# Kernel optimization log

Hardware: AMD Instinct MI355X
Metric: run time of the kernel (lower is better)

The kernel has to match this reference:

```python
import jax, jax.numpy as jnp
import numpy as np

N_ATOMS = 100_000
N_BONDS = 200_000
MAX_NB = 6
HIDDEN = 300
ATOM_FD = 133
BOND_FD = 147
DEPTH = 3
ATOMS_PER_MOL = 20
N_MOLS = N_ATOMS // ATOMS_PER_MOL


def setup_inputs() -> dict:
    key = jax.random.key(0)
    ks = jax.random.split(key, 9)
    f_atoms = jax.random.normal(ks[0], (N_ATOMS, ATOM_FD), dtype=jnp.float32)
    f_bonds = jax.random.normal(ks[1], (N_BONDS, BOND_FD), dtype=jnp.float32)
    a2b = jax.random.randint(ks[2], (N_ATOMS, MAX_NB), 0, N_BONDS, dtype=jnp.int32)
    b2a = jax.random.randint(ks[3], (N_BONDS,), 0, N_ATOMS, dtype=jnp.int32)
    b2revb = jax.random.randint(ks[4], (N_BONDS,), 0, N_BONDS, dtype=jnp.int32)
    mol_ids = (jnp.arange(N_ATOMS, dtype=jnp.int32) // ATOMS_PER_MOL).astype(jnp.int32)
    W_i = jax.random.normal(ks[5], (BOND_FD, HIDDEN), dtype=jnp.float32) * 0.05
    W_h = jax.random.normal(ks[6], (HIDDEN, HIDDEN), dtype=jnp.float32) * 0.05
    W_o = jax.random.normal(ks[7], (ATOM_FD + HIDDEN, HIDDEN), dtype=jnp.float32) * 0.05
    b_o = jax.random.normal(ks[8], (HIDDEN,), dtype=jnp.float32) * 0.05
    return {"f_atoms": f_atoms, "f_bonds": f_bonds, "a2b": a2b, "b2a": b2a,
            "b2revb": b2revb, "mol_ids": mol_ids, "W_i": W_i, "W_h": W_h,
            "W_o": W_o, "b_o": b_o}


def reference(f_atoms, f_bonds, a2b, b2a, b2revb, mol_ids, W_i, W_h, W_o, b_o):
    # input = W_i(f_bonds); message = act(input)
    inp = f_bonds @ W_i                     # [n_bonds, H]
    message = jax.nn.relu(inp)
    for _ in range(DEPTH - 1):
        # padded-neighbor gather + sum over incoming bonds per atom
        a_message = message[a2b].sum(axis=1)          # [n_atoms, H]
        # forward gather minus reverse-bond message
        m = a_message[b2a] - message[b2revb]          # [n_bonds, H]
        message = jax.nn.relu(inp + m @ W_h)          # (dropout p=0 omitted)
    # final atom readout
    a_message = message[a2b].sum(axis=1)              # [n_atoms, H]
    a_input = jnp.concatenate([f_atoms, a_message], axis=1)  # [n_atoms, atom_fd+H]
    atom_hiddens = jax.nn.relu(a_input @ W_o + b_o)   # [n_atoms, H]
    # 'mean' pooling over each molecule's atoms (contiguous equal-size scopes)
    mol_sums = jax.ops.segment_sum(atom_hiddens, mol_ids, num_segments=N_MOLS)
    return mol_sums / ATOMS_PER_MOL                   # [n_mols, H]
```

## Files before the change

### kernel.cpp

```cpp
#include <hip/hip_runtime.h>
#include <hip/hip_bf16.h>
#include <hip/hip_fp8.h>

#define N_ATOMS 100000
#define N_BONDS 200000
#define MAX_NB 6
#define HIDDEN 300
#define HP 320
#define CH 40
#define ATOM_FD 133
#define BOND_FD 147
#define N_MOLS 5000
#define APM 20

#define NT32 10
#define KKI32 10
#define KKH32 20
#define KKO32 28

using bf16 = __hip_bfloat16;
typedef __attribute__((ext_vector_type(8))) short short8v;
typedef __attribute__((ext_vector_type(4))) float float4v;
typedef __attribute__((ext_vector_type(2))) float float2v;
typedef __attribute__((ext_vector_type(16))) float float16v;
typedef unsigned int u32;
typedef unsigned short u16;
typedef unsigned char u8;

__device__ __forceinline__ float us2f(u16 u) {
    union { u32 i; float f; } v; v.i = ((u32)u) << 16; return v.f;
}
__device__ __forceinline__ u16 f2us(float f) {
    bf16 h = __float2bfloat16(f);
    return *(u16*)&h;
}
__device__ __forceinline__ u32 pack2(float a, float b) {
    return (u32)f2us(a) | ((u32)f2us(b) << 16);
}
__device__ __forceinline__ uint2 pack4(const float4v& a) {
    uint2 o; o.x = pack2(a[0], a[1]); o.y = pack2(a[2], a[3]); return o;
}

#if defined(__has_builtin)
#if __has_builtin(__builtin_amdgcn_cvt_f32_fp8) && __has_builtin(__builtin_amdgcn_cvt_pk_fp8_f32)
#define HW_FP8 1
#endif
#if __has_builtin(__builtin_amdgcn_cvt_pk_f32_fp8)
#define HW_FP8_PK 1
#endif
#endif

__device__ __forceinline__ void f8x4_to_f32(u32 p, float* o) {
#if defined(HW_FP8_PK)
    float2v lo = __builtin_amdgcn_cvt_pk_f32_fp8(p, false);
    float2v hi = __builtin_amdgcn_cvt_pk_f32_fp8(p, true);
    o[0] = lo[0]; o[1] = lo[1]; o[2] = hi[0]; o[3] = hi[1];
#elif defined(HW_FP8)
    o[0] = __builtin_amdgcn_cvt_f32_fp8(p, 0);
    o[1] = __builtin_amdgcn_cvt_f32_fp8(p, 1);
    o[2] = __builtin_amdgcn_cvt_f32_fp8(p, 2);
    o[3] = __builtin_amdgcn_cvt_f32_fp8(p, 3);
#else
#pragma unroll
    for (int i = 0; i < 4; ++i) {
        __hip_fp8_e4m3 h; h.__x = (u8)(p >> (8 * i));
        o[i] = (float)h;
    }
#endif
}
__device__ __forceinline__ u32 f32x4_to_f8(float a, float b, float c, float d) {
#ifdef HW_FP8
    u32 r = __builtin_amdgcn_cvt_pk_fp8_f32(a, b, 0u, false);
    r = __builtin_amdgcn_cvt_pk_fp8_f32(c, d, r, true);
    return r;
#else
    __hip_fp8_e4m3 ha(a), hb(b), hc(c), hd(d);
    return (u32)ha.__x | ((u32)hb.__x << 8) | ((u32)hc.__x << 16) | ((u32)hd.__x << 24);
#endif
}
__device__ __forceinline__ void f8x16_to_f32(uint4 u, float* o) {
    f8x4_to_f32(u.x, o); f8x4_to_f32(u.y, o + 4);
    f8x4_to_f32(u.z, o + 8); f8x4_to_f32(u.w, o + 12);
}
__device__ __forceinline__ u32 relu_f8x4(u32 u) {
    u32 m = (u >> 7) & 0x01010101u;
    return u & ~(m * 255u);
}
__device__ __forceinline__ uint4 relu_f8x16(uint4 u) {
    u.x = relu_f8x4(u.x); u.y = relu_f8x4(u.y);
    u.z = relu_f8x4(u.z); u.w = relu_f8x4(u.w);
    return u;
}

__global__ __launch_bounds__(64) void pack_w32(const float* __restrict__ src,
                                               short* __restrict__ dst,
                                               int Ksrc, int mode) {
    int kk = blockIdx.x / NT32, nt = blockIdx.x % NT32;
    int lane = threadIdx.x;
    int col = nt * 32 + (lane & 31);
#pragma unroll
    for (int j = 0; j < 8; ++j) {
        int k = kk * 16 + (lane >> 5) * 8 + j;
        float v = 0.f;
        if (k < Ksrc && col < HIDDEN) {
            int krow = k;
            if (mode == 2) krow = (k < HIDDEN) ? (ATOM_FD + k) : (k - HIDDEN);
            v = src[krow * HIDDEN + col];
        }
        dst[(((kk * NT32 + nt) << 6) + lane) * 8 + j] = (short)f2us(v);
    }
}

__global__ __launch_bounds__(256) void k0_zero(float* __restrict__ out) {
    int i = blockIdx.x * 256 + threadIdx.x;
    if (i < N_MOLS * HIDDEN) out[i] = 0.f;
}

__global__ __launch_bounds__(320) void k1_input(const float* __restrict__ fb,
                                                const short8v* __restrict__ WiP,
                                                u8* __restrict__ inp8) {
    __shared__ __align__(16) char sm[32 * 640];
    const int tid = threadIdx.x;
    const long base = (long)blockIdx.x * 32;
    const float4* src4 = (const float4*)(fb + base * BOND_FD);
#pragma unroll
    for (int it = 0; it < 4; ++it) {
        int idx = tid + it * 320;
        if (idx < 1176) {
            float4 v = src4[idx];
            int f = idx * 4;
#pragma unroll
            for (int e = 0; e < 4; ++e) {
                int g = f + e;
                int r = g / BOND_FD, c = g - r * BOND_FD;
                int byte = r * 320 + c * 2;
                *(u16*)(sm + (byte ^ ((r & 7) << 4))) = f2us(((const float*)&v)[e]);
            }
        }
    }
    for (int i = tid; i < 32 * 13; i += 320) {
        int r = i / 13, c = BOND_FD + i % 13;
        int byte = r * 320 + c * 2;
        *(u16*)(sm + (byte ^ ((r & 7) << 4))) = 0;
    }
    __syncthreads();

    const int lane = tid & 63, wave = tid >> 6;
    const int row = lane & 31, hi = lane >> 5;
    const int nt0 = wave * 2;
    float16v acc0, acc1;
#pragma unroll
    for (int q = 0; q < 16; ++q) { acc0[q] = 0.f; acc1[q] = 0.f; }
    for (int kk = 0; kk < KKI32; ++kk) {
        int byte = row * 320 + kk * 32 + hi * 16;
        short8v a = *(const short8v*)(sm + (byte ^ ((row & 7) << 4)));
        short8v w0 = WiP[((kk * NT32 + nt0) << 6) + lane];
        short8v w1 = WiP[((kk * NT32 + nt0 + 1) << 6) + lane];
        acc0 = __builtin_amdgcn_mfma_f32_32x32x16_bf16(w0, a, acc0, 0, 0, 0);
        acc1 = __builtin_amdgcn_mfma_f32_32x32x16_bf16(w1, a, acc1, 0, 0, 0);
    }
    __syncthreads();
#pragma unroll
    for (int t = 0; t < 2; ++t) {
#pragma unroll
        for (int q = 0; q < 4; ++q) {
            int colb = (nt0 + t) * 32 + q * 8 + hi * 4;
            float a0 = (t == 0 ? acc0[4 * q + 0] : acc1[4 * q + 0]);
            float a1 = (t == 0 ? acc0[4 * q + 1] : acc1[4 * q + 1]);
            float a2 = (t == 0 ? acc0[4 * q + 2] : acc1[4 * q + 2]);
            float a3 = (t == 0 ? acc0[4 * q + 3] : acc1[4 * q + 3]);
            *(u32*)(sm + row * 336 + colb) = f32x4_to_f8(a0, a1, a2, a3);
        }
    }
    __syncthreads();
#pragma unroll
    for (int it = 0; it < 2; ++it) {
        int i = tid + it * 320;
        int r = i / 20, c = i % 20;
        uint4 v = *(const uint4*)(sm + r * 336 + c * 16);
        ((uint4*)(inp8 + (base + r) * 320))[c] = v;
    }
}

template<int RELU>
__global__ __launch_bounds__(256, 8) void k2_gather(const u8* __restrict__ src,
                                                    const int* __restrict__ a2b,
                                                    u8* __restrict__ dst) {
    int id = blockIdx.x * 256 + threadIdx.x;
    int atom = id / 10, c2 = id % 10;
    if (atom >= N_ATOMS) return;
    const int* nb = a2b + atom * MAX_NB;
    float s[32];
#pragma unroll
    for (int q = 0; q < 32; ++q) s[q] = 0.f;
#pragma unroll
    for (int j = 0; j < MAX_NB; ++j) {
        const uint4* rp = (const uint4*)(src + (long)nb[j] * 320);
        uint4 u0 = rp[2 * c2];
        uint4 u1 = rp[2 * c2 + 1];
        if (RELU) { u0 = relu_f8x16(u0); u1 = relu_f8x16(u1); }
        float v[16];
        f8x16_to_f32(u0, v);
#pragma unroll
        for (int q = 0; q < 16; ++q) s[q] += v[q];
        f8x16_to_f32(u1, v);
#pragma unroll
        for (int q = 0; q < 16; ++q) s[16 + q] += v[q];
    }
    uint4 o0, o1;
    o0.x = f32x4_to_f8(s[0], s[1], s[2], s[3]);
    o0.y = f32x4_to_f8(s[4], s[5], s[6], s[7]);
    o0.z = f32x4_to_f8(s[8], s[9], s[10], s[11]);
    o0.w = f32x4_to_f8(s[12], s[13], s[14], s[15]);
    o1.x = f32x4_to_f8(s[16], s[17], s[18], s[19]);
    o1.y = f32x4_to_f8(s[20], s[21], s[22], s[23]);
    o1.z = f32x4_to_f8(s[24], s[25], s[26], s[27]);
    o1.w = f32x4_to_f8(s[28], s[29], s[30], s[31]);
    uint4* dp = (uint4*)(dst + (long)atom * 320);
    dp[2 * c2] = o0;
    dp[2 * c2 + 1] = o1;
}

template<int RELUSRC>
__global__ __launch_bounds__(320) void kzf_update(const u8* __restrict__ inp8,
                                                  const u8* __restrict__ AM,
                                                  const u8* __restrict__ msgsrc,
                                                  const int* __restrict__ b2a,
                                                  const int* __restrict__ b2revb,
                                                  const short8v* __restrict__ WhP,
                                                  u8* __restrict__ msgdst) {
    __shared__ __align__(16) char sm[32 * 640];
    const int tid = threadIdx.x;
    const long base = (long)blockIdx.x * 32;

#pragma unroll
    for (int it = 0; it < 2; ++it) {
        int i = tid + it * 320;
        int r = i / 20, c = i % 20;
        long b = base + r;
        int ia = b2a[b], ir = b2revb[b];
        uint4 ua = ((const uint4*)(AM + (long)ia * 320))[c];
        uint4 um = ((const uint4*)(msgsrc + (long)ir * 320))[c];
        if (RELUSRC) um = relu_f8x16(um);
        float av[16], mv[16];
        f8x16_to_f32(ua, av);
        f8x16_to_f32(um, mv);
        uint4 o0, o1;
        o0.x = pack2(av[0] - mv[0], av[1] - mv[1]);
        o0.y = pack2(av[2] - mv[2], av[3] - mv[3]);
        o0.z = pack2(av[4] - mv[4], av[5] - mv[5]);
        o0.w = pack2(av[6] - mv[6], av[7] - mv[7]);
        o1.x = pack2(av[8] - mv[8], av[9] - mv[9]);
        o1.y = pack2(av[10] - mv[10], av[11] - mv[11]);
        o1.z = pack2(av[12] - mv[12], av[13] - mv[13]);
        o1.w = pack2(av[14] - mv[14], av[15] - mv[15]);
        int byte = r * 640 + c * 32;
        int swz = (r & 7) << 4;
        *(uint4*)(sm + (byte ^ swz)) = o0;
        *(uint4*)(sm + ((byte + 16) ^ swz)) = o1;
    }
    __syncthreads();

    const int lane = tid & 63, wave = tid >> 6;
    const int row = lane & 31, hi = lane >> 5;
    const int nt0 = wave * 2;
    float16v acc0, acc1;
#pragma unroll
    for (int q = 0; q < 16; ++q) { acc0[q] = 0.f; acc1[q] = 0.f; }
    for (int kk = 0; kk < KKH32; ++kk) {
        int byte = row * 640 + kk * 32 + hi * 16;
        short8v a = *(const short8v*)(sm + (byte ^ ((row & 7) << 4)));
        short8v w0 = WhP[((kk * NT32 + nt0) << 6) + lane];
        short8v w1 = WhP[((kk * NT32 + nt0 + 1) << 6) + lane];
        acc0 = __builtin_amdgcn_mfma_f32_32x32x16_bf16(w0, a, acc0, 0, 0, 0);
        acc1 = __builtin_amdgcn_mfma_f32_32x32x16_bf16(w1, a, acc1, 0, 0, 0);
    }
    __syncthreads();
#pragma unroll
    for (int t = 0; t < 2; ++t) {
#pragma unroll
        for (int q = 0; q < 4; ++q) {
            int colb = (nt0 + t) * 32 + q * 8 + hi * 4;
            u32 u = *(const u32*)(inp8 + (base + row) * 320 + colb);
            float iv[4];
            f8x4_to_f32(u, iv);
            float a0 = (t == 0 ? acc0[4 * q + 0] : acc1[4 * q + 0]);
            float a1 = (t == 0 ? acc0[4 * q + 1] : acc1[4 * q + 1]);
            float a2 = (t == 0 ? acc0[4 * q + 2] : acc1[4 * q + 2]);
            float a3 = (t == 0 ? acc0[4 * q + 3] : acc1[4 * q + 3]);
            float v0 = fmaxf(a0 + iv[0], 0.f);
            float v1 = fmaxf(a1 + iv[1], 0.f);
            float v2 = fmaxf(a2 + iv[2], 0.f);
            float v3 = fmaxf(a3 + iv[3], 0.f);
            *(u32*)(sm + row * 336 + colb) = f32x4_to_f8(v0, v1, v2, v3);
        }
    }
    __syncthreads();
#pragma unroll
    for (int it = 0; it < 2; ++it) {
        int i = tid + it * 320;
        int r = i / 20, c = i % 20;
        uint4 v = *(const uint4*)(sm + r * 336 + c * 16);
        ((uint4*)(msgdst + (base + r) * 320))[c] = v;
    }
}

__global__ __launch_bounds__(320) void k4_gemm(const float* __restrict__ fa,
                                               const u8* __restrict__ AM,
                                               const short8v* __restrict__ WoP,
                                               const float* __restrict__ bo,
                                               float* __restrict__ out) {
    __shared__ __align__(16) char sm[32 * 896];
    const int tid = threadIdx.x;
    const long base = (long)blockIdx.x * 32;
#pragma unroll
    for (int it = 0; it < 2; ++it) {
        int i = tid + it * 320;
        if (i < 608) {
            int row = i / 19, c = i % 19;
            uint4 u = ((const uint4*)(AM + (base + row) * 320))[c];
            float s[16];
            f8x16_to_f32(u, s);
            uint4 o0, o1;
            o0.x = pack2(s[0], s[1]);  o0.y = pack2(s[2], s[3]);
            o0.z = pack2(s[4], s[5]);  o0.w = pack2(s[6], s[7]);
            o1.x = pack2(s[8], s[9]);  o1.y = pack2(s[10], s[11]);
            o1.z = pack2(s[12], s[13]); o1.w = pack2(s[14], s[15]);
            int byte = row * 896 + c * 32;
            int swz = (row & 7) << 4;
            *(uint4*)(sm + (byte ^ swz)) = o0;
            if (c < 18) {
                *(uint4*)(sm + ((byte + 16) ^ swz)) = o1;
            } else {
                *(uint2*)(sm + ((byte + 16) ^ swz)) = make_uint2(o1.x, o1.y);
            }
        }
    }
    const float4* src4 = (const float4*)(fa + base * ATOM_FD);
#pragma unroll
    for (int it = 0; it < 4; ++it) {
        int idx = tid + it * 320;
        if (idx < 1064) {
            float4 v = src4[idx];
            int f = idx * 4;
#pragma unroll
            for (int e = 0; e < 4; ++e) {
                int g = f + e;
                int r = g / ATOM_FD, c2 = g - r * ATOM_FD;
                int byte = r * 896 + (HIDDEN + c2) * 2;
                *(u16*)(sm + (byte ^ ((r & 7) << 4))) = f2us(((const float*)&v)[e]);
            }
        }
    }
    for (int i = tid; i < 480; i += 320) {
        int r = i / 15, c2 = ATOM_FD + i % 15;
        int byte = r * 896 + (HIDDEN + c2) * 2;
        *(u16*)(sm + (byte ^ ((r & 7) << 4))) = 0;
    }
    __syncthreads();

    const int lane = tid & 63, wave = tid >> 6;
    const int row = lane & 31, hi = lane >> 5;
    const int nt0 = wave * 2;
    float16v acc0, acc1;
#pragma unroll
    for (int q = 0; q < 16; ++q) { acc0[q] = 0.f; acc1[q] = 0.f; }
    for (int kk = 0; kk < KKO32; ++kk) {
        int byte = row * 896 + kk * 32 + hi * 16;
        short8v a = *(const short8v*)(sm + (byte ^ ((row & 7) << 4)));
        short8v w0 = WoP[((kk * NT32 + nt0) << 6) + lane];
        short8v w1 = WoP[((kk * NT32 + nt0 + 1) << 6) + lane];
        acc0 = __builtin_amdgcn_mfma_f32_32x32x16_bf16(w0, a, acc0, 0, 0, 0);
        acc1 = __builtin_amdgcn_mfma_f32_32x32x16_bf16(w1, a, acc1, 0, 0, 0);
    }
    __syncthreads();
#pragma unroll
    for (int t = 0; t < 2; ++t) {
#pragma unroll
        for (int q = 0; q < 4; ++q) {
            int colb = (nt0 + t) * 32 + q * 8 + hi * 4;
            float4v v;
#pragma unroll
            for (int d = 0; d < 4; ++d) {
                float bias = (colb + d < HIDDEN) ? bo[colb + d] : 0.f;
                float av = (t == 0 ? acc0[4 * q + d] : acc1[4 * q + d]);
                v[d] = fmaxf(av + bias, 0.f);
            }
            int byte = row * 640 + colb * 2;
            *(uint2*)(sm + (byte ^ ((row & 7) << 4))) = pack4(v);
        }
    }
    __syncthreads();
    const int mfirst = (int)(base / APM);
    const int mlast = (int)((base + 31) / APM);
    const int nseg = mlast - mfirst + 1;
    for (int idx = tid; idx < nseg * HIDDEN; idx += 320) {
        int s = idx / HIDDEN, col = idx % HIDDEN;
        int m = mfirst + s;
        long a0 = (long)m * APM; if (a0 < base) a0 = base;
        long a1 = (long)(m + 1) * APM; if (a1 > base + 32) a1 = base + 32;
        float sum = 0.f;
        for (long a = a0; a < a1; ++a) {
            int r = (int)(a - base);
            int byte = r * 640 + col * 2;
            sum += us2f(*(const u16*)(sm + (byte ^ ((r & 7) << 4))));
        }
        atomicAdd(out + (long)m * HIDDEN + col, sum * (1.f / APM));
    }
}

extern "C" void kernel_launch(void* const* d_in, const int* in_sizes, int n_in,
                              void* d_out, int out_size, void* d_ws, size_t ws_size,
                              hipStream_t stream) {
    const float* f_atoms = (const float*)d_in[0];
    const float* f_bonds = (const float*)d_in[1];
    const int* a2b = (const int*)d_in[2];
    const int* b2a = (const int*)d_in[3];
    const int* b2revb = (const int*)d_in[4];
    const float* Wi = (const float*)d_in[6];
    const float* Wh = (const float*)d_in[7];
    const float* Wo = (const float*)d_in[8];
    const float* bo = (const float*)d_in[9];
    float* out = (float*)d_out;

    char* ws = (char*)d_ws;
    size_t off = 0;
    auto alloc = [&](size_t bytes) {
        void* p = ws + off;
        off = (off + bytes + 255) & ~(size_t)255;
        return p;
    };
    u8* inp8  = (u8*)alloc((size_t)N_BONDS * 320);
    u8* msgA  = (u8*)alloc((size_t)N_BONDS * 320);
    u8* msgB  = (u8*)alloc((size_t)N_BONDS * 320);
    u8* AM    = (u8*)alloc((size_t)N_ATOMS * 320);
    short* WiP32 = (short*)alloc((size_t)KKI32 * NT32 * 64 * 8 * sizeof(short));
    short* WhP32 = (short*)alloc((size_t)KKH32 * NT32 * 64 * 8 * sizeof(short));
    short* WoP32 = (short*)alloc((size_t)KKO32 * NT32 * 64 * 8 * sizeof(short));

    pack_w32<<<KKI32 * NT32, 64, 0, stream>>>(Wi, WiP32, BOND_FD, 0);
    pack_w32<<<KKH32 * NT32, 64, 0, stream>>>(Wh, WhP32, HIDDEN, 0);
    pack_w32<<<KKO32 * NT32, 64, 0, stream>>>(Wo, WoP32, ATOM_FD + HIDDEN, 2);
    k0_zero<<<(N_MOLS * HIDDEN + 255) / 256, 256, 0, stream>>>(out);

    k1_input<<<N_BONDS / 32, 320, 0, stream>>>(f_bonds, (const short8v*)WiP32, inp8);

    const int g2 = (N_ATOMS * 10 + 255) / 256;
    k2_gather<1><<<g2, 256, 0, stream>>>(inp8, a2b, AM);
    kzf_update<1><<<N_BONDS / 32, 320, 0, stream>>>(inp8, AM, inp8, b2a, b2revb,
                                                    (const short8v*)WhP32, msgA);
    k2_gather<0><<<g2, 256, 0, stream>>>(msgA, a2b, AM);
    kzf_update<0><<<N_BONDS / 32, 320, 0, stream>>>(inp8, AM, msgA, b2a, b2revb,
                                                    (const short8v*)WhP32, msgB);
    k2_gather<0><<<g2, 256, 0, stream>>>(msgB, a2b, AM);
    k4_gemm<<<N_ATOMS / 32, 320, 0, stream>>>(f_atoms, AM,
                                              (const short8v*)WoP32, bo, out);
}
```

Measured before the change: 448.4 us.

## Widen update kernel to 64 bonds per block and fuse final gather into readout

The message-update kernel now processes 64 bonds per block instead of 32, so each Wh weight fragment loaded from global memory feeds four MFMAs instead of two, which halves weight traffic per bond. The final neighbor gather-sum is folded into the readout GEMM kernel, which removes one launch and the write and re-read of the atom message buffer. In exchange the update kernel uses twice the LDS and more accumulator registers, which may lower occupancy, and the readout kernel now does scattered gathers before its GEMM.

```diff
diff --git a/kernel.cpp b/kernel.cpp
--- a/kernel.cpp
+++ b/kernel.cpp
@@ -229,12 +229,12 @@
                                                   const int* __restrict__ b2revb,
                                                   const short8v* __restrict__ WhP,
                                                   u8* __restrict__ msgdst) {
-    __shared__ __align__(16) char sm[32 * 640];
+    __shared__ __align__(16) char sm[64 * 640];
     const int tid = threadIdx.x;
-    const long base = (long)blockIdx.x * 32;
-
-#pragma unroll
-    for (int it = 0; it < 2; ++it) {
+    const long base = (long)blockIdx.x * 64;
+
+#pragma unroll
+    for (int it = 0; it < 4; ++it) {
         int i = tid + it * 320;
         int r = i / 20, c = i % 20;
         long b = base + r;
@@ -262,42 +262,61 @@
     __syncthreads();
 
     const int lane = tid & 63, wave = tid >> 6;
-    const int row = lane & 31, hi = lane >> 5;
+    const int row0 = lane & 31, hi = lane >> 5;
     const int nt0 = wave * 2;
-    float16v acc0, acc1;
-#pragma unroll
-    for (int q = 0; q < 16; ++q) { acc0[q] = 0.f; acc1[q] = 0.f; }
+    float16v acc00, acc01, acc10, acc11;
+#pragma unroll
+    for (int q = 0; q < 16; ++q) {
+        acc00[q] = 0.f; acc01[q] = 0.f; acc10[q] = 0.f; acc11[q] = 0.f;
+    }
     for (int kk = 0; kk < KKH32; ++kk) {
-        int byte = row * 640 + kk * 32 + hi * 16;
-        short8v a = *(const short8v*)(sm + (byte ^ ((row & 7) << 4)));
+        int b0 = row0 * 640 + kk * 32 + hi * 16;
+        int r1 = 32 + row0;
+        int b1 = r1 * 640 + kk * 32 + hi * 16;
+        short8v a0 = *(const short8v*)(sm + (b0 ^ ((row0 & 7) << 4)));
+        short8v a1 = *(const short8v*)(sm + (b1 ^ ((r1 & 7) << 4)));
         short8v w0 = WhP[((kk * NT32 + nt0) << 6) + lane];
         short8v w1 = WhP[((kk * NT32 + nt0 + 1) << 6) + lane];
-        acc0 = __builtin_amdgcn_mfma_f32_32x32x16_bf16(w0, a, acc0, 0, 0, 0);
-        acc1 = __builtin_amdgcn_mfma_f32_32x32x16_bf16(w1, a, acc1, 0, 0, 0);
-    }
-    __syncthreads();
-#pragma unroll
-    for (int t = 0; t < 2; ++t) {
-#pragma unroll
-        for (int q = 0; q < 4; ++q) {
-            int colb = (nt0 + t) * 32 + q * 8 + hi * 4;
-            u32 u = *(const u32*)(inp8 + (base + row) * 320 + colb);
-            float iv[4];
-            f8x4_to_f32(u, iv);
-            float a0 = (t == 0 ? acc0[4 * q + 0] : acc1[4 * q + 0]);
-            float a1 = (t == 0 ? acc0[4 * q + 1] : acc1[4 * q + 1]);
-            float a2 = (t == 0 ? acc0[4 * q + 2] : acc1[4 * q + 2]);
-            float a3 = (t == 0 ? acc0[4 * q + 3] : acc1[4 * q + 3]);
-            float v0 = fmaxf(a0 + iv[0], 0.f);
-            float v1 = fmaxf(a1 + iv[1], 0.f);
-            float v2 = fmaxf(a2 + iv[2], 0.f);
-            float v3 = fmaxf(a3 + iv[3], 0.f);
-            *(u32*)(sm + row * 336 + colb) = f32x4_to_f8(v0, v1, v2, v3);
-        }
-    }
-    __syncthreads();
-#pragma unroll
-    for (int it = 0; it < 2; ++it) {
+        acc00 = __builtin_amdgcn_mfma_f32_32x32x16_bf16(w0, a0, acc00, 0, 0, 0);
+        acc01 = __builtin_amdgcn_mfma_f32_32x32x16_bf16(w1, a0, acc01, 0, 0, 0);
+        acc10 = __builtin_amdgcn_mfma_f32_32x32x16_bf16(w0, a1, acc10, 0, 0, 0);
+        acc11 = __builtin_amdgcn_mfma_f32_32x32x16_bf16(w1, a1, acc11, 0, 0, 0);
+    }
+    __syncthreads();
+#pragma unroll
+    for (int rg = 0; rg < 2; ++rg) {
+        int row = rg * 32 + row0;
+#pragma unroll
+        for (int t = 0; t < 2; ++t) {
+#pragma unroll
+            for (int q = 0; q < 4; ++q) {
+                int colb = (nt0 + t) * 32 + q * 8 + hi * 4;
+                u32 u = *(const u32*)(inp8 + (base + row) * 320 + colb);
+                float iv[4];
+                f8x4_to_f32(u, iv);
+                float a0, a1, a2, a3;
+                if (rg == 0) {
+                    a0 = (t == 0 ? acc00[4 * q + 0] : acc01[4 * q + 0]);
+                    a1 = (t == 0 ? acc00[4 * q + 1] : acc01[4 * q + 1]);
+                    a2 = (t == 0 ? acc00[4 * q + 2] : acc01[4 * q + 2]);
+                    a3 = (t == 0 ? acc00[4 * q + 3] : acc01[4 * q + 3]);
+                } else {
+                    a0 = (t == 0 ? acc10[4 * q + 0] : acc11[4 * q + 0]);
+                    a1 = (t == 0 ? acc10[4 * q + 1] : acc11[4 * q + 1]);
+                    a2 = (t == 0 ? acc10[4 * q + 2] : acc11[4 * q + 2]);
+                    a3 = (t == 0 ? acc10[4 * q + 3] : acc11[4 * q + 3]);
+                }
+                float v0 = fmaxf(a0 + iv[0], 0.f);
+                float v1 = fmaxf(a1 + iv[1], 0.f);
+                float v2 = fmaxf(a2 + iv[2], 0.f);
+                float v3 = fmaxf(a3 + iv[3], 0.f);
+                *(u32*)(sm + row * 336 + colb) = f32x4_to_f8(v0, v1, v2, v3);
+            }
+        }
+    }
+    __syncthreads();
+#pragma unroll
+    for (int it = 0; it < 4; ++it) {
         int i = tid + it * 320;
         int r = i / 20, c = i % 20;
         uint4 v = *(const uint4*)(sm + r * 336 + c * 16);
@@ -306,7 +325,8 @@
 }
 
 __global__ __launch_bounds__(320) void k4_gemm(const float* __restrict__ fa,
-                                               const u8* __restrict__ AM,
+                                               const u8* __restrict__ msg,
+                                               const int* __restrict__ a2b,
                                                const short8v* __restrict__ WoP,
                                                const float* __restrict__ bo,
                                                float* __restrict__ out) {
@@ -318,9 +338,18 @@
         int i = tid + it * 320;
         if (i < 608) {
             int row = i / 19, c = i % 19;
-            uint4 u = ((const uint4*)(AM + (base + row) * 320))[c];
-            float s[16];
+            long atom = base + row;
+            const int* nb = a2b + atom * MAX_NB;
+            float s[16], v[16];
+            uint4 u = ((const uint4*)(msg + (long)nb[0] * 320))[c];
             f8x16_to_f32(u, s);
+#pragma unroll
+            for (int j = 1; j < MAX_NB; ++j) {
+                uint4 uj = ((const uint4*)(msg + (long)nb[j] * 320))[c];
+                f8x16_to_f32(uj, v);
+#pragma unroll
+                for (int q = 0; q < 16; ++q) s[q] += v[q];
+            }
             uint4 o0, o1;
             o0.x = pack2(s[0], s[1]);  o0.y = pack2(s[2], s[3]);
             o0.z = pack2(s[4], s[5]);  o0.w = pack2(s[6], s[7]);
@@ -447,12 +476,11 @@
 
     const int g2 = (N_ATOMS * 10 + 255) / 256;
     k2_gather<1><<<g2, 256, 0, stream>>>(inp8, a2b, AM);
-    kzf_update<1><<<N_BONDS / 32, 320, 0, stream>>>(inp8, AM, inp8, b2a, b2revb,
+    kzf_update<1><<<N_BONDS / 64, 320, 0, stream>>>(inp8, AM, inp8, b2a, b2revb,
                                                     (const short8v*)WhP32, msgA);
     k2_gather<0><<<g2, 256, 0, stream>>>(msgA, a2b, AM);
-    kzf_update<0><<<N_BONDS / 32, 320, 0, stream>>>(inp8, AM, msgA, b2a, b2revb,
+    kzf_update<0><<<N_BONDS / 64, 320, 0, stream>>>(inp8, AM, msgA, b2a, b2revb,
                                                     (const short8v*)WhP32, msgB);
-    k2_gather<0><<<g2, 256, 0, stream>>>(msgB, a2b, AM);
-    k4_gemm<<<N_ATOMS / 32, 320, 0, stream>>>(f_atoms, AM,
+    k4_gemm<<<N_ATOMS / 32, 320, 0, stream>>>(f_atoms, msgB, a2b,
                                               (const short8v*)WoP32, bo, out);
 }
```

Result: no change. 442.5 us (-1.3%).
